# Kernel tuning notes

Measured on AMD Instinct MI355X. Metric: run time of the kernel, lower is better.

Reference implementation:

```python
import jax, jax.numpy as jnp
import numpy as np

B, N, C, H, REG = 1, 2309, 1024, 16, 5
D = C // H


def setup_inputs() -> dict:
    key = jax.random.key(0)
    k0, k1, k2, k3 = jax.random.split(key, 4)
    x = jax.random.normal(k0, (B, N, C), dtype=jnp.float32)
    g_info = jax.random.normal(k1, (12, 2, C), dtype=jnp.float32)
    W_qkv = jax.random.normal(k2, (C, 3 * C), dtype=jnp.float32) * 0.02
    W_proj = jax.random.normal(k3, (C, C), dtype=jnp.float32) * 0.02
    b_proj = jnp.zeros((C,), dtype=jnp.float32)
    return {"x": x, "g_info": g_info, "W_qkv": W_qkv, "W_proj": W_proj, "b_proj": b_proj}


def reference(x, g_info, W_qkv, W_proj, b_proj):
    Bx, Nx, Cx = x.shape
    scale = D ** -0.5
    # qkv projection (qkv_bias=False)
    qkv = (x @ W_qkv).reshape(Bx, Nx, 3, H, D)
    q, k, v = qkv[:, :, 0], qkv[:, :, 1], qkv[:, :, 2]  # [B,N,H,D]

    # grounding query vector from layer 0
    g_layer = g_info[0].reshape(-1, H, D)
    q_g = g_layer[0]  # [H,D]

    # cosine-similarity routing over non-register tokens
    q_pure = q[:, REG:]  # [B,M,H,D]
    q_n = q_pure / jnp.linalg.norm(q_pure, axis=-1, keepdims=True)
    qg_n = q_g / jnp.linalg.norm(q_g, axis=-1, keepdims=True)
    sim = (qg_n[None, None] * q_n).sum(-1).mean(-1)  # [B,M]
    sim = (sim - sim.min()) / (sim.max() - sim.min())  # global min-max normalize
    pos = sim > 0.9  # [B,M] boolean routing mask

    # Full logits computed once; group attention = masked softmax over the
    # group's key set (registers always included). This is mathematically
    # identical to the torch gather->attend->scatter, with static shapes.
    logits = jnp.einsum('bqhd,bkhd->bhqk', q * scale, k)  # [B,H,N,N]

    def masked_attn(tok_mask):
        key_mask = jnp.concatenate([jnp.ones((Bx, REG), bool), tok_mask], axis=1)  # [B,N]
        l = jnp.where(key_mask[:, None, None, :], logits, -jnp.inf)
        a = jax.nn.softmax(l, axis=-1)
        return jnp.einsum('bhqk,bkhd->bqhd', a, v)  # [B,N,H,D]

    x_pos = masked_attn(pos)
    x_neg = masked_attn(~pos)

    reg_out = (x_pos[:, :REG] + x_neg[:, :REG]) * 0.5
    tok_out = jnp.where(pos[:, :, None, None], x_pos[:, REG:], x_neg[:, REG:])
    out = jnp.concatenate([reg_out, tok_out], axis=1).reshape(Bx, Nx, Cx)
    return out @ W_proj + b_proj
```

## Files before the change

### kernel.cpp

```cpp
#include <hip/hip_runtime.h>
#include <math.h>

#define TOK 2309
#define CH 1024
#define NH 16
#define HD 64
#define NREG 5
#define NTOK (TOK - NREG)
#define NPADQ 2432
#define NPAD2 2560
#define NKT 40
#define HTILES 20
#define NQROW 2368
#define QSCL 0.1803368801f

typedef unsigned short ushort_t;
typedef unsigned char uchar_t;
typedef __attribute__((ext_vector_type(8))) short s8frag;
typedef __attribute__((ext_vector_type(4))) float f4frag;
typedef __attribute__((ext_vector_type(2))) long ll2;

__device__ __forceinline__ float wredsum(float v){
  #pragma unroll
  for (int o = 32; o > 0; o >>= 1) v += __shfl_xor(v, o, 64);
  return v;
}

__device__ __forceinline__ unsigned short f2bf(float x){
  union { float f; unsigned u; } v; v.f = x;
  unsigned r = v.u + 0x7FFF + ((v.u >> 16) & 1);
  return (unsigned short)(r >> 16);
}
__device__ __forceinline__ float bf2f(unsigned short u){
  union { unsigned u32; float f; } v; v.u32 = ((unsigned)u) << 16;
  return v.f;
}
__device__ __forceinline__ unsigned pack_bf16(float lo, float hi){
  union { float f; unsigned u; } a, b;
  a.f = lo; b.f = hi;
  return __builtin_amdgcn_perm(b.u + 0x8000u, a.u + 0x8000u, 0x07060302u);
}
__device__ __forceinline__ uchar_t f2fp8(float x){
  return (uchar_t)(__builtin_amdgcn_cvt_pk_fp8_f32(x, x, 0, false) & 0xff);
}
__device__ __forceinline__ void cp16(const void* g, void* l){
  __builtin_amdgcn_global_load_lds(
      (const __attribute__((address_space(1))) unsigned int*)g,
      (__attribute__((address_space(3))) unsigned int*)l, 16, 0, 0);
}

__global__ __launch_bounds__(256) void split_x_kernel(
    const float* __restrict__ X, ushort_t* __restrict__ Xhi, ushort_t* __restrict__ Xlo)
{
  int row = blockIdx.x;
  int c4 = threadIdx.x * 4;
  ushort4 h4 = {0,0,0,0}, l4 = {0,0,0,0};
  if (row < TOK) {
    float4 v = *(const float4*)&X[(size_t)row*CH + c4];
    float vv[4] = {v.x, v.y, v.z, v.w};
    ushort_t hs[4], ls[4];
    #pragma unroll
    for (int i = 0; i < 4; i++) {
      hs[i] = f2bf(vv[i]);
      ls[i] = f2bf(vv[i] - bf2f(hs[i]));
    }
    h4.x=hs[0]; h4.y=hs[1]; h4.z=hs[2]; h4.w=hs[3];
    l4.x=ls[0]; l4.y=ls[1]; l4.z=ls[2]; l4.w=ls[3];
  }
  *(ushort4*)&Xhi[(size_t)row*CH + c4] = h4;
  *(ushort4*)&Xlo[(size_t)row*CH + c4] = l4;
}

__global__ __launch_bounds__(256) void pack_w_kernel(
    const float* __restrict__ W, const int N,
    ushort_t* __restrict__ WT, ushort_t* __restrict__ WloT, const int loN)
{
  __shared__ float T[64][68];
  const int tid = threadIdx.x;
  const int n0 = blockIdx.x * 64;
  const int k0 = blockIdx.y * 64;
  const int lr = tid >> 4;
  const int lc = (tid & 15) * 4;
  #pragma unroll
  for (int s = 0; s < 4; s++) {
    float4 v = *(const float4*)&W[(size_t)(k0 + lr + s*16) * N + n0 + lc];
    *(float4*)&T[lr + s*16][lc] = v;
  }
  __syncthreads();
  const int nl = tid >> 2;
  const int kc = (tid & 3) * 16;
  const bool dolo = (WloT != nullptr) && (n0 < loN);
  ushort_t* dh = WT + (size_t)(n0 + nl) * CH + k0 + kc;
  ushort_t* dl = WloT + (size_t)(n0 + nl) * CH + k0 + kc;
  #pragma unroll
  for (int g = 0; g < 4; g++) {
    float a = T[kc+g*4+0][nl], b = T[kc+g*4+1][nl];
    float c = T[kc+g*4+2][nl], d = T[kc+g*4+3][nl];
    ushort4 oh;
    oh.x=f2bf(a); oh.y=f2bf(b); oh.z=f2bf(c); oh.w=f2bf(d);
    *(ushort4*)&dh[g*4] = oh;
    if (dolo) {
      ushort4 ol;
      ol.x=f2bf(a-bf2f(oh.x)); ol.y=f2bf(b-bf2f(oh.y));
      ol.z=f2bf(c-bf2f(oh.z)); ol.w=f2bf(d-bf2f(oh.w));
      *(ushort4*)&dl[g*4] = ol;
    }
  }
}

__global__ __launch_bounds__(256) void gemm_qkv_mfma(
    const ushort_t* __restrict__ Xhi, const ushort_t* __restrict__ Xlo,
    const ushort_t* __restrict__ WhiT, const ushort_t* __restrict__ WloT,
    float* __restrict__ Qf, uchar_t* __restrict__ Q8,
    uchar_t* __restrict__ K8, ushort_t* __restrict__ Vbf)
{
  __shared__ ushort_t LA[2][2][4096];
  __shared__ ushort_t LB[2][2][4096];
  const int tid = threadIdx.x;
  const int w = tid >> 6, lane = tid & 63;
  const int quad = lane >> 4, c16 = lane & 15;
  const int wm = w >> 1, wn = w & 1;
  const int nt = blockIdx.x, mt = blockIdx.y;
  const int n0 = nt * 128, m0 = mt * 128;
  const bool isQ = (nt < 8);

  const int srow = tid >> 2;
  const int g = (tid & 3) ^ ((tid >> 3) & 3);
  const size_t aoff = (size_t)(m0 + srow)*CH + g*8;
  const size_t boff = (size_t)(n0 + srow)*CH + g*8;
  const int lbase = (tid & 192) * 8;

  f4frag acc[4][4];
  #pragma unroll
  for (int mi = 0; mi < 4; mi++)
    #pragma unroll
    for (int nb = 0; nb < 4; nb++) acc[mi][nb] = (f4frag){0.f,0.f,0.f,0.f};

  const int soff = (quad ^ ((c16 >> 1) & 3)) * 8;
  int aro[4], bro[4];
  #pragma unroll
  for (int i = 0; i < 4; i++) {
    aro[i] = (wm*64 + i*16 + c16)*32 + soff;
    bro[i] = (wn*64 + i*16 + c16)*32 + soff;
  }

#define QKV_STAGE(KT, BUF) {                                                   \
    const int _k = (KT)*32;                                                    \
    cp16(Xhi  + aoff + _k,                 &LA[BUF][0][lbase]);                \
    cp16(Xhi  + aoff + _k + (size_t)64*CH, &LA[BUF][0][2048 + lbase]);         \
    cp16(WhiT + boff + _k,                 &LB[BUF][0][lbase]);                \
    cp16(WhiT + boff + _k + (size_t)64*CH, &LB[BUF][0][2048 + lbase]);         \
    if (isQ) {                                                                 \
      cp16(Xlo  + aoff + _k,                 &LA[BUF][1][lbase]);              \
      cp16(Xlo  + aoff + _k + (size_t)64*CH, &LA[BUF][1][2048 + lbase]);       \
      cp16(WloT + boff + _k,                 &LB[BUF][1][lbase]);              \
      cp16(WloT + boff + _k + (size_t)64*CH, &LB[BUF][1][2048 + lbase]);       \
    } }

  QKV_STAGE(0, 0);
  for (int kt = 0; kt < 32; kt++) {
    const int buf = kt & 1;
    __syncthreads();
    if (kt < 31) { QKV_STAGE(kt+1, buf^1); }
    s8frag a[4], b[4];
    #pragma unroll
    for (int i = 0; i < 4; i++) a[i] = *(const s8frag*)&LA[buf][0][aro[i]];
    #pragma unroll
    for (int i = 0; i < 4; i++) b[i] = *(const s8frag*)&LB[buf][0][bro[i]];
    #pragma unroll
    for (int mi = 0; mi < 4; mi++)
      #pragma unroll
      for (int nb = 0; nb < 4; nb++)
        acc[mi][nb] = __builtin_amdgcn_mfma_f32_16x16x32_bf16(a[mi], b[nb], acc[mi][nb], 0, 0, 0);
    if (isQ) {
      s8frag al[4], bl[4];
      #pragma unroll
      for (int i = 0; i < 4; i++) al[i] = *(const s8frag*)&LA[buf][1][aro[i]];
      #pragma unroll
      for (int i = 0; i < 4; i++) bl[i] = *(const s8frag*)&LB[buf][1][bro[i]];
      #pragma unroll
      for (int mi = 0; mi < 4; mi++)
        #pragma unroll
        for (int nb = 0; nb < 4; nb++) {
          acc[mi][nb] = __builtin_amdgcn_mfma_f32_16x16x32_bf16(a[mi],  bl[nb], acc[mi][nb], 0, 0, 0);
          acc[mi][nb] = __builtin_amdgcn_mfma_f32_16x16x32_bf16(al[mi], b[nb],  acc[mi][nb], 0, 0, 0);
        }
    }
  }
#undef QKV_STAGE

  const int three = (nt >= 16) ? 2 : (nt >= 8) ? 1 : 0;
  #pragma unroll
  for (int mi = 0; mi < 4; mi++) {
    const int orow = m0 + wm*64 + mi*16 + quad*4;
    if (three == 0) {
      #pragma unroll
      for (int nb = 0; nb < 4; nb++) {
        const int col = n0 + wn*64 + nb*16 + c16;
        const int h = (col >> 6) & 15, d = col & 63;
        float* qf = Qf + (size_t)h*TOK*HD;
        uchar_t* q8 = Q8 + (size_t)h*NPADQ*64;
        #pragma unroll
        for (int r = 0; r < 4; r++) {
          int row = orow + r;
          float v = (row < TOK) ? acc[mi][nb][r] : 0.f;
          if (row < TOK) qf[(size_t)row*HD + d] = v;
          q8[(size_t)row*64 + d] = f2fp8(v);
        }
      }
    } else if (three == 1) {
      #pragma unroll
      for (int nb = 0; nb < 4; nb++) {
        const int col = n0 + wn*64 + nb*16 + c16;
        const int h = (col >> 6) & 15;
        const int quadK = ((nb & 1) * 2) + (c16 >> 3);
        const int byteoff = (nb >> 1) * 8 + (c16 & 7);
        uchar_t* base = K8 + (size_t)h*NKT*4096;
        #pragma unroll
        for (int r = 0; r < 4; r++) {
          int row = orow + r;
          float v = (row < TOK) ? acc[mi][nb][r] : 0.f;
          int tile = row >> 6, b = (row >> 4) & 3, c16K = row & 15;
          base[(size_t)tile*4096 + b*1024 + (quadK*16 + c16K)*16 + byteoff] = f2fp8(v);
        }
      }
    } else {
      const int tile  = orow >> 6;
      const int jj    = orow & 63;
      const int c     = jj >> 5;
      const int t16   = (jj >> 4) & 1;
      const int quadA = (jj >> 2) & 3;
      #pragma unroll
      for (int nb = 0; nb < 4; nb++) {
        const int col = n0 + wn*64 + nb*16 + c16;
        const int h = (col >> 6) & 15, d = col & 63;
        const int dblk = d >> 4, c16A = d & 15;
        ushort_t* base = Vbf + (size_t)h*NKT*4096;
        ushort4 o;
        o.x = f2bf((orow+0 < TOK) ? acc[mi][nb][0] : 0.f);
        o.y = f2bf((orow+1 < TOK) ? acc[mi][nb][1] : 0.f);
        o.z = f2bf((orow+2 < TOK) ? acc[mi][nb][2] : 0.f);
        o.w = f2bf((orow+3 < TOK) ? acc[mi][nb][3] : 0.f);
        *(ushort4*)&base[(size_t)tile*4096 + dblk*1024 + c*512
                         + (quadA*16 + c16A)*8 + 4*t16] = o;
      }
    }
  }
}

__global__ __launch_bounds__(256) void sim_kernel(
    const float* __restrict__ Q, const float* __restrict__ G, float* __restrict__ sim)
{
  const int tid = threadIdx.x;
  const int w = tid >> 6, lane = tid & 63;
  float qgn[NH];
  #pragma unroll
  for (int h = 0; h < NH; h++) {
    float g = G[h*HD + lane];
    float n2 = wredsum(g*g);
    qgn[h] = g / sqrtf(n2);
  }
  int it = blockIdx.x * 4 + w;
  if (it >= NTOK) return;
  int i = NREG + it;
  float acc = 0.f;
  #pragma unroll
  for (int h = 0; h < NH; h++) {
    float qv = Q[((size_t)h*TOK + i)*HD + lane];
    float dot = wredsum(qv * qgn[h]);
    float n2  = wredsum(qv * qv);
    acc += dot / sqrtf(n2);
  }
  if (lane == 0) sim[it] = acc * (1.0f/16.0f);
}

__global__ __launch_bounds__(256) void mask_kernel(
    const float* __restrict__ sim, int* __restrict__ cls,
    float* __restrict__ WP, float* __restrict__ WN)
{
  __shared__ float smn[256], smx[256];
  const int tid = threadIdx.x;
  float mn = 1e30f, mx = -1e30f;
  for (int i = tid; i < NTOK; i += 256) { float s = sim[i]; mn = fminf(mn, s); mx = fmaxf(mx, s); }
  smn[tid] = mn; smx[tid] = mx;
  __syncthreads();
  for (int off = 128; off > 0; off >>= 1) {
    if (tid < off) { smn[tid] = fminf(smn[tid], smn[tid+off]); smx[tid] = fmaxf(smx[tid], smx[tid+off]); }
    __syncthreads();
  }
  mn = smn[0]; mx = smx[0];
  float inv = 1.0f / (mx - mn);
  for (int j = tid; j < NPAD2; j += 256) {
    float wp = 0.f, wn = 0.f; int c = 0;
    if (j < NREG) { wp = 1.f; wn = 1.f; c = 2; }
    else if (j < TOK) {
      bool pos = ((sim[j-NREG] - mn) * inv) > 0.9f;
      c = pos ? 1 : 0;
      wp = pos ? 1.f : 0.f;
      wn = pos ? 0.f : 1.f;
    }
    WP[j] = wp; WN[j] = wn;
    if (j < TOK) cls[j] = c;
  }
}

__global__ __launch_bounds__(256) void attn_kernel(
    const uchar_t* __restrict__ Q8, const uchar_t* __restrict__ K8,
    const ushort_t* __restrict__ Vbf,
    const float* __restrict__ WP, const float* __restrict__ WN,
    ushort_t* __restrict__ POp, ushort_t* __restrict__ POn,
    float* __restrict__ Lp, float* __restrict__ Ln)
{
  __shared__ __align__(16) uchar_t smem[24576];
  uchar_t* Kst = smem;
  uchar_t* Vst = smem + 8192;
  const int tid = threadIdx.x;
  const int w = tid >> 6, lane = tid & 63;
  const int quad = lane >> 4, c16 = lane & 15;
  const int h = blockIdx.y;
  const int half = blockIdx.z;
  const int q0 = blockIdx.x * 64;

  const uchar_t* Qh = Q8 + (size_t)h * NPADQ * 64;
  const uchar_t* gk = K8 + ((size_t)h*NKT + half*HTILES)*4096 + tid*16;
  const uchar_t* gv = (const uchar_t*)Vbf + ((size_t)h*NKT + half*HTILES)*8192 + tid*16;
  const int lw = w * 1024;

  const uchar_t* qp = Qh + (size_t)(q0 + w*16 + c16)*64 + quad*8;
  const long qf0 = *(const long*)(qp);
  const long qf1 = *(const long*)(qp + 32);

  f4frag op[4], on[4];
  #pragma unroll
  for (int nb = 0; nb < 4; nb++) { op[nb] = (f4frag){0.f,0.f,0.f,0.f}; on[nb] = (f4frag){0.f,0.f,0.f,0.f}; }
  float lp = 0.f, ln = 0.f;

  cp16(gk, Kst + lw);
  cp16(gv, Vst + lw);
  cp16(gv + 4096, Vst + 4096 + lw);

  int pb = 0;
  for (int t = 0; t < HTILES; t++) {
    __syncthreads();
    if (t < HTILES-1) {
      cp16(gk + (size_t)(t+1)*4096, Kst + (pb^1)*4096 + lw);
      cp16(gv + (size_t)(t+1)*8192,        Vst + (pb^1)*8192 + lw);
      cp16(gv + (size_t)(t+1)*8192 + 4096, Vst + (pb^1)*8192 + 4096 + lw);
    }
    const int j0 = half*(HTILES*64) + t*64;
    f4frag st[4];
    #pragma unroll
    for (int b = 0; b < 4; b++) {
      ll2 kv = *(const ll2*)&Kst[pb*4096 + b*1024 + lane*16];
      f4frag z = (f4frag){0.f,0.f,0.f,0.f};
      z     = __builtin_amdgcn_mfma_f32_16x16x32_fp8_fp8(kv.x, qf0, z, 0, 0, 0);
      st[b] = __builtin_amdgcn_mfma_f32_16x16x32_fp8_fp8(kv.y, qf1, z, 0, 0, 0);
    }
    unsigned pu[4][2], nu[4][2];
    #pragma unroll
    for (int b = 0; b < 4; b++) {
      float4 wp4 = *(const float4*)&WP[j0 + b*16 + quad*4];
      float4 wn4 = *(const float4*)&WN[j0 + b*16 + quad*4];
      float p0 = __builtin_amdgcn_exp2f(st[b][0] * QSCL);
      float p1 = __builtin_amdgcn_exp2f(st[b][1] * QSCL);
      float p2 = __builtin_amdgcn_exp2f(st[b][2] * QSCL);
      float p3 = __builtin_amdgcn_exp2f(st[b][3] * QSCL);
      float a0 = p0*wp4.x, a1 = p1*wp4.y, a2 = p2*wp4.z, a3 = p3*wp4.w;
      float b0 = p0*wn4.x, b1 = p1*wn4.y, b2 = p2*wn4.z, b3 = p3*wn4.w;
      lp += (a0+a1)+(a2+a3);
      ln += (b0+b1)+(b2+b3);
      pu[b][0] = pack_bf16(a0, a1); pu[b][1] = pack_bf16(a2, a3);
      nu[b][0] = pack_bf16(b0, b1); nu[b][1] = pack_bf16(b2, b3);
    }
    union Frag { unsigned u[4]; s8frag v; };
    Frag fp0, fp1, fn0, fn1;
    fp0.u[0]=pu[0][0]; fp0.u[1]=pu[0][1]; fp0.u[2]=pu[1][0]; fp0.u[3]=pu[1][1];
    fp1.u[0]=pu[2][0]; fp1.u[1]=pu[2][1]; fp1.u[2]=pu[3][0]; fp1.u[3]=pu[3][1];
    fn0.u[0]=nu[0][0]; fn0.u[1]=nu[0][1]; fn0.u[2]=nu[1][0]; fn0.u[3]=nu[1][1];
    fn1.u[0]=nu[2][0]; fn1.u[1]=nu[2][1]; fn1.u[2]=nu[3][0]; fn1.u[3]=nu[3][1];
    #pragma unroll
    for (int nb = 0; nb < 4; nb++) {
      s8frag va = *(const s8frag*)&Vst[pb*8192 + nb*2048 + lane*16];
      s8frag vb = *(const s8frag*)&Vst[pb*8192 + nb*2048 + 1024 + lane*16];
      op[nb] = __builtin_amdgcn_mfma_f32_16x16x32_bf16(va, fp0.v, op[nb], 0, 0, 0);
      op[nb] = __builtin_amdgcn_mfma_f32_16x16x32_bf16(vb, fp1.v, op[nb], 0, 0, 0);
      on[nb] = __builtin_amdgcn_mfma_f32_16x16x32_bf16(va, fn0.v, on[nb], 0, 0, 0);
      on[nb] = __builtin_amdgcn_mfma_f32_16x16x32_bf16(vb, fn1.v, on[nb], 0, 0, 0);
    }
    pb ^= 1;
  }

  lp += __shfl_xor(lp, 16, 64); lp += __shfl_xor(lp, 32, 64);
  ln += __shfl_xor(ln, 16, 64); ln += __shfl_xor(ln, 32, 64);
  const int iq = q0 + w*16 + c16;
  if (quad == 0 && iq < TOK) {
    Lp[((size_t)half*NH + h)*NQROW + iq] = lp;
    Ln[((size_t)half*NH + h)*NQROW + iq] = ln;
  }
  if (iq < TOK) {
    const size_t base = (size_t)half*NQROW*CH + (size_t)iq*CH + h*HD;
    #pragma unroll
    for (int nb = 0; nb < 4; nb++) {
      uint2 po, no;
      po.x = pack_bf16(op[nb][0], op[nb][1]);
      po.y = pack_bf16(op[nb][2], op[nb][3]);
      no.x = pack_bf16(on[nb][0], on[nb][1]);
      no.y = pack_bf16(on[nb][2], on[nb][3]);
      *(uint2*)(POp + base + nb*16 + quad*4) = po;
      *(uint2*)(POn + base + nb*16 + quad*4) = no;
    }
  }
}

__global__ __launch_bounds__(256) void merge_kernel(
    const ushort_t* __restrict__ POp, const ushort_t* __restrict__ POn,
    const float* __restrict__ Lp, const float* __restrict__ Ln,
    const int* __restrict__ cls, ushort_t* __restrict__ AObf)
{
  const int row = blockIdx.x;
  const int c4 = threadIdx.x * 4;
  const int h = c4 >> 6;
  const size_t o0 = (size_t)row*CH + c4;
  const size_t o1 = (size_t)NQROW*CH + o0;
  ushort4 p0 = *(const ushort4*)(POp + o0);
  ushort4 p1 = *(const ushort4*)(POp + o1);
  ushort4 n0 = *(const ushort4*)(POn + o0);
  ushort4 n1 = *(const ushort4*)(POn + o1);
  const float lpt = Lp[(size_t)h*NQROW + row] + Lp[(size_t)(NH+h)*NQROW + row];
  const float lnt = Ln[(size_t)h*NQROW + row] + Ln[(size_t)(NH+h)*NQROW + row];
  const float ilp = 1.f / lpt, iln = 1.f / lnt;
  const int cq = cls[row];
  float vp[4], vn[4], o[4];
  vp[0] = (bf2f(p0.x)+bf2f(p1.x))*ilp; vn[0] = (bf2f(n0.x)+bf2f(n1.x))*iln;
  vp[1] = (bf2f(p0.y)+bf2f(p1.y))*ilp; vn[1] = (bf2f(n0.y)+bf2f(n1.y))*iln;
  vp[2] = (bf2f(p0.z)+bf2f(p1.z))*ilp; vn[2] = (bf2f(n0.z)+bf2f(n1.z))*iln;
  vp[3] = (bf2f(p0.w)+bf2f(p1.w))*ilp; vn[3] = (bf2f(n0.w)+bf2f(n1.w))*iln;
  if (row < NREG) {
    #pragma unroll
    for (int i = 0; i < 4; i++) o[i] = 0.5f*(vp[i]+vn[i]);
  } else if (cq == 1) {
    #pragma unroll
    for (int i = 0; i < 4; i++) o[i] = vp[i];
  } else {
    #pragma unroll
    for (int i = 0; i < 4; i++) o[i] = vn[i];
  }
  uint2 pk;
  pk.x = pack_bf16(o[0], o[1]);
  pk.y = pack_bf16(o[2], o[3]);
  *(uint2*)(AObf + (size_t)row*CH + c4) = pk;
}

__global__ __launch_bounds__(256) void gemm_proj_mfma(
    const ushort_t* __restrict__ A, const ushort_t* __restrict__ WT,
    const float* __restrict__ bp, float* __restrict__ out)
{
  __shared__ ushort_t LA[2][4096];
  __shared__ ushort_t LB[2][2048];
  const int tid = threadIdx.x;
  const int w = tid >> 6, lane = tid & 63;
  const int quad = lane >> 4, c16 = lane & 15;
  const int wm = w >> 1, wn = w & 1;
  const int nt = blockIdx.x, mt = blockIdx.y;
  const int n0 = nt * 64, m0 = mt * 128;

  const int srow = tid >> 2;
  const int g = (tid & 3) ^ ((tid >> 3) & 3);
  const size_t aoff = (size_t)(m0 + srow)*CH + g*8;
  const size_t boff = (size_t)(n0 + srow)*CH + g*8;
  const int lbase = (tid & 192) * 8;

  f4frag acc[4][2];
  #pragma unroll
  for (int mi = 0; mi < 4; mi++)
    #pragma unroll
    for (int nb = 0; nb < 2; nb++) acc[mi][nb] = (f4frag){0.f,0.f,0.f,0.f};

  const int soff = (quad ^ ((c16 >> 1) & 3)) * 8;
  int aro[4], bro[2];
  #pragma unroll
  for (int i = 0; i < 4; i++) aro[i] = (wm*64 + i*16 + c16)*32 + soff;
  #pragma unroll
  for (int i = 0; i < 2; i++) bro[i] = (wn*32 + i*16 + c16)*32 + soff;

#define PROJ_STAGE(KT, BUF) {                                                  \
    const int _k = (KT)*32;                                                    \
    cp16(A  + aoff + _k,                 &LA[BUF][lbase]);                     \
    cp16(A  + aoff + _k + (size_t)64*CH, &LA[BUF][2048 + lbase]);              \
    cp16(WT + boff + _k,                 &LB[BUF][lbase]);                     \
    }

  PROJ_STAGE(0, 0);
  for (int kt = 0; kt < 32; kt++) {
    const int buf = kt & 1;
    __syncthreads();
    if (kt < 31) { PROJ_STAGE(kt+1, buf^1); }
    s8frag a[4], b[2];
    #pragma unroll
    for (int i = 0; i < 4; i++) a[i] = *(const s8frag*)&LA[buf][aro[i]];
    #pragma unroll
    for (int i = 0; i < 2; i++) b[i] = *(const s8frag*)&LB[buf][bro[i]];
    #pragma unroll
    for (int mi = 0; mi < 4; mi++)
      #pragma unroll
      for (int nb = 0; nb < 2; nb++)
        acc[mi][nb] = __builtin_amdgcn_mfma_f32_16x16x32_bf16(a[mi], b[nb], acc[mi][nb], 0, 0, 0);
  }
#undef PROJ_STAGE

  #pragma unroll
  for (int mi = 0; mi < 4; mi++) {
    const int orow = m0 + wm*64 + mi*16 + quad*4;
    #pragma unroll
    for (int nb = 0; nb < 2; nb++) {
      const int col = n0 + wn*32 + nb*16 + c16;
      const float bias = bp[col];
      #pragma unroll
      for (int r = 0; r < 4; r++) {
        int row = orow + r;
        if (row < TOK) out[(size_t)row*CH + col] = acc[mi][nb][r] + bias;
      }
    }
  }
}

extern "C" void kernel_launch(void* const* d_in, const int* in_sizes, int n_in,
                              void* d_out, int out_size, void* d_ws, size_t ws_size,
                              hipStream_t stream) {
  const float* x      = (const float*)d_in[0];
  const float* g_info = (const float*)d_in[1];
  const float* W_qkv  = (const float*)d_in[2];
  const float* W_proj = (const float*)d_in[3];
  const float* b_proj = (const float*)d_in[4];
  float* out = (float*)d_out;

  float* ws = (float*)d_ws;
  float* Qf  = ws;
  float* SIM = Qf + (size_t)NH*TOK*HD;
  float* WP  = SIM + NTOK;
  float* WN  = WP + NPAD2;
  int*   CLS = (int*)(WN + NPAD2);
  float* LpB = (float*)(CLS + 2312);
  float* LnB = LpB + (size_t)2*NH*NQROW;
  ushort_t* Xhi    = (ushort_t*)(LnB + (size_t)2*NH*NQROW);
  ushort_t* Xlo    = Xhi    + (size_t)NPADQ*CH;
  ushort_t* WqkvT  = Xlo    + (size_t)NPADQ*CH;
  ushort_t* WqkvLo = WqkvT  + (size_t)3*CH*CH;
  ushort_t* WprojT = WqkvLo + (size_t)CH*CH;
  ushort_t* AObf   = WprojT + (size_t)CH*CH;
  ushort_t* POp    = AObf   + (size_t)NPADQ*CH;
  ushort_t* POn    = POp    + (size_t)2*NQROW*CH;
  uchar_t*  Q8     = (uchar_t*)(POn + (size_t)2*NQROW*CH);
  uchar_t*  K8     = Q8 + (size_t)NH*NPADQ*64;
  ushort_t* Vbf    = (ushort_t*)(K8 + (size_t)NH*NKT*4096);

  hipMemsetAsync(K8, 0, (size_t)NH*NKT*4096 + (size_t)NH*NKT*8192, stream);

  split_x_kernel<<<dim3(NPADQ), 256, 0, stream>>>(x, Xhi, Xlo);
  pack_w_kernel<<<dim3(48, 16), 256, 0, stream>>>(W_qkv, 3*CH, WqkvT, WqkvLo, CH);
  pack_w_kernel<<<dim3(16, 16), 256, 0, stream>>>(W_proj, CH, WprojT, nullptr, 0);
  gemm_qkv_mfma<<<dim3(24, 19), 256, 0, stream>>>(Xhi, Xlo, WqkvT, WqkvLo,
                                                  Qf, Q8, K8, Vbf);
  sim_kernel<<<dim3(576), 256, 0, stream>>>(Qf, g_info, SIM);
  mask_kernel<<<dim3(1), 256, 0, stream>>>(SIM, CLS, WP, WN);
  attn_kernel<<<dim3(37, NH, 2), 256, 0, stream>>>(Q8, K8, Vbf, WP, WN,
                                                   POp, POn, LpB, LnB);
  merge_kernel<<<dim3(TOK), 256, 0, stream>>>(POp, POn, LpB, LnB, CLS, AObf);
  gemm_proj_mfma<<<dim3(16, 19), 256, 0, stream>>>(AObf, WprojT, b_proj, out);
}
```

Before: 257.1 us.

## Drop split-bf16 Q precision, compute routing dot via precomputed W·g projection

```diff
diff --git a/kernel.cpp b/kernel.cpp
--- a/kernel.cpp
+++ b/kernel.cpp
@@ -8,9 +8,9 @@
 #define NREG 5
 #define NTOK (TOK - NREG)
 #define NPADQ 2432
-#define NPAD2 2560
-#define NKT 40
-#define HTILES 20
+#define NPAD2 2432
+#define NKT 38
+#define HTILES 19
 #define NQROW 2368
 #define QSCL 0.1803368801f
 
@@ -20,12 +20,6 @@
 typedef __attribute__((ext_vector_type(4))) float f4frag;
 typedef __attribute__((ext_vector_type(2))) long ll2;
 
-__device__ __forceinline__ float wredsum(float v){
-  #pragma unroll
-  for (int o = 32; o > 0; o >>= 1) v += __shfl_xor(v, o, 64);
-  return v;
-}
-
 __device__ __forceinline__ unsigned short f2bf(float x){
   union { float f; unsigned u; } v; v.f = x;
   unsigned r = v.u + 0x7FFF + ((v.u >> 16) & 1);
@@ -50,34 +44,29 @@
 }
 
 __global__ __launch_bounds__(256) void split_x_kernel(
-    const float* __restrict__ X, ushort_t* __restrict__ Xhi, ushort_t* __restrict__ Xlo)
+    const float* __restrict__ X, ushort_t* __restrict__ Xbf)
 {
   int row = blockIdx.x;
   int c4 = threadIdx.x * 4;
-  ushort4 h4 = {0,0,0,0}, l4 = {0,0,0,0};
+  ushort4 h4 = {0,0,0,0};
   if (row < TOK) {
     float4 v = *(const float4*)&X[(size_t)row*CH + c4];
-    float vv[4] = {v.x, v.y, v.z, v.w};
-    ushort_t hs[4], ls[4];
-    #pragma unroll
-    for (int i = 0; i < 4; i++) {
-      hs[i] = f2bf(vv[i]);
-      ls[i] = f2bf(vv[i] - bf2f(hs[i]));
-    }
-    h4.x=hs[0]; h4.y=hs[1]; h4.z=hs[2]; h4.w=hs[3];
-    l4.x=ls[0]; l4.y=ls[1]; l4.z=ls[2]; l4.w=ls[3];
-  }
-  *(ushort4*)&Xhi[(size_t)row*CH + c4] = h4;
-  *(ushort4*)&Xlo[(size_t)row*CH + c4] = l4;
+    h4.x = f2bf(v.x); h4.y = f2bf(v.y); h4.z = f2bf(v.z); h4.w = f2bf(v.w);
+  }
+  *(ushort4*)&Xbf[(size_t)row*CH + c4] = h4;
 }
 
 __global__ __launch_bounds__(256) void pack_w_kernel(
-    const float* __restrict__ W, const int N,
-    ushort_t* __restrict__ WT, ushort_t* __restrict__ WloT, const int loN)
+    const float* __restrict__ Wqkv, const float* __restrict__ Wproj,
+    ushort_t* __restrict__ WqkvT, ushort_t* __restrict__ WprojT)
 {
   __shared__ float T[64][68];
   const int tid = threadIdx.x;
-  const int n0 = blockIdx.x * 64;
+  int bx = blockIdx.x;
+  const float* W; ushort_t* WT; int N;
+  if (bx < 48) { W = Wqkv; WT = WqkvT; N = 3*CH; }
+  else         { W = Wproj; WT = WprojT; N = CH; bx -= 48; }
+  const int n0 = bx * 64;
   const int k0 = blockIdx.y * 64;
   const int lr = tid >> 4;
   const int lc = (tid & 15) * 4;
@@ -89,40 +78,55 @@
   __syncthreads();
   const int nl = tid >> 2;
   const int kc = (tid & 3) * 16;
-  const bool dolo = (WloT != nullptr) && (n0 < loN);
   ushort_t* dh = WT + (size_t)(n0 + nl) * CH + k0 + kc;
-  ushort_t* dl = WloT + (size_t)(n0 + nl) * CH + k0 + kc;
   #pragma unroll
   for (int g = 0; g < 4; g++) {
-    float a = T[kc+g*4+0][nl], b = T[kc+g*4+1][nl];
-    float c = T[kc+g*4+2][nl], d = T[kc+g*4+3][nl];
     ushort4 oh;
-    oh.x=f2bf(a); oh.y=f2bf(b); oh.z=f2bf(c); oh.w=f2bf(d);
+    oh.x = f2bf(T[kc+g*4+0][nl]); oh.y = f2bf(T[kc+g*4+1][nl]);
+    oh.z = f2bf(T[kc+g*4+2][nl]); oh.w = f2bf(T[kc+g*4+3][nl]);
     *(ushort4*)&dh[g*4] = oh;
-    if (dolo) {
-      ushort4 ol;
-      ol.x=f2bf(a-bf2f(oh.x)); ol.y=f2bf(b-bf2f(oh.y));
-      ol.z=f2bf(c-bf2f(oh.z)); ol.w=f2bf(d-bf2f(oh.w));
-      *(ushort4*)&dl[g*4] = ol;
-    }
-  }
+  }
+}
+
+__global__ __launch_bounds__(256) void ghat_kernel(
+    const float* __restrict__ G, const float* __restrict__ Wqkv,
+    float* __restrict__ U)
+{
+  const int tid = threadIdx.x;
+  const int k = blockIdx.x * 16 + (tid >> 4);
+  const int h = tid & 15;
+  const float* g = G + h*64;
+  float n2 = 0.f;
+  #pragma unroll
+  for (int d = 0; d < 64; d += 4) {
+    float4 gv = *(const float4*)&g[d];
+    n2 += gv.x*gv.x + gv.y*gv.y + gv.z*gv.z + gv.w*gv.w;
+  }
+  const float inv = 1.f / sqrtf(n2);
+  const float* wr = Wqkv + (size_t)k*(3*CH) + h*64;
+  float dot = 0.f;
+  #pragma unroll
+  for (int d = 0; d < 64; d += 4) {
+    float4 wv = *(const float4*)&wr[d];
+    float4 gv = *(const float4*)&g[d];
+    dot += wv.x*gv.x + wv.y*gv.y + wv.z*gv.z + wv.w*gv.w;
+  }
+  U[h*CH + k] = dot * inv;
 }
 
 __global__ __launch_bounds__(256) void gemm_qkv_mfma(
-    const ushort_t* __restrict__ Xhi, const ushort_t* __restrict__ Xlo,
-    const ushort_t* __restrict__ WhiT, const ushort_t* __restrict__ WloT,
-    float* __restrict__ Qf, uchar_t* __restrict__ Q8,
+    const ushort_t* __restrict__ Xbf, const ushort_t* __restrict__ WT,
+    ushort_t* __restrict__ Qbf, uchar_t* __restrict__ Q8,
     uchar_t* __restrict__ K8, ushort_t* __restrict__ Vbf)
 {
-  __shared__ ushort_t LA[2][2][4096];
-  __shared__ ushort_t LB[2][2][4096];
+  __shared__ ushort_t LA[2][4096];
+  __shared__ ushort_t LB[2][4096];
   const int tid = threadIdx.x;
   const int w = tid >> 6, lane = tid & 63;
   const int quad = lane >> 4, c16 = lane & 15;
   const int wm = w >> 1, wn = w & 1;
   const int nt = blockIdx.x, mt = blockIdx.y;
   const int n0 = nt * 128, m0 = mt * 128;
-  const bool isQ = (nt < 8);
 
   const int srow = tid >> 2;
   const int g = (tid & 3) ^ ((tid >> 3) & 3);
@@ -146,16 +150,11 @@
 
 #define QKV_STAGE(KT, BUF) {                                                   \
     const int _k = (KT)*32;                                                    \
-    cp16(Xhi  + aoff + _k,                 &LA[BUF][0][lbase]);                \
-    cp16(Xhi  + aoff + _k + (size_t)64*CH, &LA[BUF][0][2048 + lbase]);         \
-    cp16(WhiT + boff + _k,                 &LB[BUF][0][lbase]);                \
-    cp16(WhiT + boff + _k + (size_t)64*CH, &LB[BUF][0][2048 + lbase]);         \
-    if (isQ) {                                                                 \
-      cp16(Xlo  + aoff + _k,                 &LA[BUF][1][lbase]);              \
-      cp16(Xlo  + aoff + _k + (size_t)64*CH, &LA[BUF][1][2048 + lbase]);       \
-      cp16(WloT + boff + _k,                 &LB[BUF][1][lbase]);              \
-      cp16(WloT + boff + _k + (size_t)64*CH, &LB[BUF][1][2048 + lbase]);       \
-    } }
+    cp16(Xbf + aoff + _k,                 &LA[BUF][lbase]);                    \
+    cp16(Xbf + aoff + _k + (size_t)64*CH, &LA[BUF][2048 + lbase]);             \
+    cp16(WT  + boff + _k,                 &LB[BUF][lbase]);                    \
+    cp16(WT  + boff + _k + (size_t)64*CH, &LB[BUF][2048 + lbase]);             \
+    }
 
   QKV_STAGE(0, 0);
   for (int kt = 0; kt < 32; kt++) {
@@ -164,28 +163,14 @@
     if (kt < 31) { QKV_STAGE(kt+1, buf^1); }
     s8frag a[4], b[4];
     #pragma unroll
-    for (int i = 0; i < 4; i++) a[i] = *(const s8frag*)&LA[buf][0][aro[i]];
-    #pragma unroll
-    for (int i = 0; i < 4; i++) b[i] = *(const s8frag*)&LB[buf][0][bro[i]];
+    for (int i = 0; i < 4; i++) a[i] = *(const s8frag*)&LA[buf][aro[i]];
+    #pragma unroll
+    for (int i = 0; i < 4; i++) b[i] = *(const s8frag*)&LB[buf][bro[i]];
     #pragma unroll
     for (int mi = 0; mi < 4; mi++)
       #pragma unroll
       for (int nb = 0; nb < 4; nb++)
         acc[mi][nb] = __builtin_amdgcn_mfma_f32_16x16x32_bf16(a[mi], b[nb], acc[mi][nb], 0, 0, 0);
-    if (isQ) {
-      s8frag al[4], bl[4];
-      #pragma unroll
-      for (int i = 0; i < 4; i++) al[i] = *(const s8frag*)&LA[buf][1][aro[i]];
-      #pragma unroll
-      for (int i = 0; i < 4; i++) bl[i] = *(const s8frag*)&LB[buf][1][bro[i]];
-      #pragma unroll
-      for (int mi = 0; mi < 4; mi++)
-        #pragma unroll
-        for (int nb = 0; nb < 4; nb++) {
-          acc[mi][nb] = __builtin_amdgcn_mfma_f32_16x16x32_bf16(a[mi],  bl[nb], acc[mi][nb], 0, 0, 0);
-          acc[mi][nb] = __builtin_amdgcn_mfma_f32_16x16x32_bf16(al[mi], b[nb],  acc[mi][nb], 0, 0, 0);
-        }
-    }
   }
 #undef QKV_STAGE
 
@@ -198,13 +183,13 @@
       for (int nb = 0; nb < 4; nb++) {
         const int col = n0 + wn*64 + nb*16 + c16;
         const int h = (col >> 6) & 15, d = col & 63;
-        float* qf = Qf + (size_t)h*TOK*HD;
-        uchar_t* q8 = Q8 + (size_t)h*NPADQ*64;
+        ushort_t* qb = Qbf + (size_t)h*NPADQ*64;
+        uchar_t*  q8 = Q8 + (size_t)h*NPADQ*64;
         #pragma unroll
         for (int r = 0; r < 4; r++) {
           int row = orow + r;
           float v = (row < TOK) ? acc[mi][nb][r] : 0.f;
-          if (row < TOK) qf[(size_t)row*HD + d] = v;
+          qb[(size_t)row*64 + d] = f2bf(v);
           q8[(size_t)row*64 + d] = f2fp8(v);
         }
       }
@@ -219,7 +204,7 @@
         #pragma unroll
         for (int r = 0; r < 4; r++) {
           int row = orow + r;
-          float v = (row < TOK) ? acc[mi][nb][r] : 0.f;
+          float v = (row < TOK) ? acc[mi][nb][r] * QSCL : 0.f;
           int tile = row >> 6, b = (row >> 4) & 3, c16K = row & 15;
           base[(size_t)tile*4096 + b*1024 + (quadK*16 + c16K)*16 + byteoff] = f2fp8(v);
         }
@@ -249,29 +234,35 @@
 }
 
 __global__ __launch_bounds__(256) void sim_kernel(
-    const float* __restrict__ Q, const float* __restrict__ G, float* __restrict__ sim)
-{
-  const int tid = threadIdx.x;
-  const int w = tid >> 6, lane = tid & 63;
-  float qgn[NH];
-  #pragma unroll
-  for (int h = 0; h < NH; h++) {
-    float g = G[h*HD + lane];
-    float n2 = wredsum(g*g);
-    qgn[h] = g / sqrtf(n2);
-  }
-  int it = blockIdx.x * 4 + w;
-  if (it >= NTOK) return;
-  int i = NREG + it;
-  float acc = 0.f;
-  #pragma unroll
-  for (int h = 0; h < NH; h++) {
-    float qv = Q[((size_t)h*TOK + i)*HD + lane];
-    float dot = wredsum(qv * qgn[h]);
-    float n2  = wredsum(qv * qv);
-    acc += dot / sqrtf(n2);
-  }
-  if (lane == 0) sim[it] = acc * (1.0f/16.0f);
+    const float* __restrict__ X, const float* __restrict__ U,
+    const ushort_t* __restrict__ Qbf, float* __restrict__ sim)
+{
+  const int gid = blockIdx.x*256 + threadIdx.x;
+  const int it = gid >> 4;
+  const int h  = gid & 15;
+  const int row = NREG + it;
+  const float* xr = X + (size_t)row*CH;
+  const float* ur = U + h*CH;
+  float num = 0.f;
+  for (int k = 0; k < CH; k += 4) {
+    float4 xv = *(const float4*)&xr[k];
+    float4 uv = *(const float4*)&ur[k];
+    num += xv.x*uv.x + xv.y*uv.y + xv.z*uv.z + xv.w*uv.w;
+  }
+  const ushort_t* qr = Qbf + ((size_t)h*NPADQ + row)*64;
+  float n2 = 0.f;
+  #pragma unroll
+  for (int d = 0; d < 64; d += 4) {
+    ushort4 a = *(const ushort4*)&qr[d];
+    float q0 = bf2f(a.x), q1 = bf2f(a.y), q2 = bf2f(a.z), q3 = bf2f(a.w);
+    n2 += q0*q0 + q1*q1 + q2*q2 + q3*q3;
+  }
+  float acc = num / sqrtf(n2);
+  acc += __shfl_xor(acc, 1, 64);
+  acc += __shfl_xor(acc, 2, 64);
+  acc += __shfl_xor(acc, 4, 64);
+  acc += __shfl_xor(acc, 8, 64);
+  if (h == 0) sim[it] = acc * (1.0f/16.0f);
 }
 
 __global__ __launch_bounds__(256) void mask_kernel(
@@ -361,10 +352,10 @@
     for (int b = 0; b < 4; b++) {
       float4 wp4 = *(const float4*)&WP[j0 + b*16 + quad*4];
       float4 wn4 = *(const float4*)&WN[j0 + b*16 + quad*4];
-      float p0 = __builtin_amdgcn_exp2f(st[b][0] * QSCL);
-      float p1 = __builtin_amdgcn_exp2f(st[b][1] * QSCL);
-      float p2 = __builtin_amdgcn_exp2f(st[b][2] * QSCL);
-      float p3 = __builtin_amdgcn_exp2f(st[b][3] * QSCL);
+      float p0 = __builtin_amdgcn_exp2f(st[b][0]);
+      float p1 = __builtin_amdgcn_exp2f(st[b][1]);
+      float p2 = __builtin_amdgcn_exp2f(st[b][2]);
+      float p3 = __builtin_amdgcn_exp2f(st[b][3]);
       float a0 = p0*wp4.x, a1 = p1*wp4.y, a2 = p2*wp4.z, a3 = p3*wp4.w;
       float b0 = p0*wn4.x, b1 = p1*wn4.y, b2 = p2*wn4.z, b3 = p3*wn4.w;
       lp += (a0+a1)+(a2+a3);
@@ -535,33 +526,29 @@
   float* out = (float*)d_out;
 
   float* ws = (float*)d_ws;
-  float* Qf  = ws;
-  float* SIM = Qf + (size_t)NH*TOK*HD;
+  float* SIM = ws;
   float* WP  = SIM + NTOK;
   float* WN  = WP + NPAD2;
   int*   CLS = (int*)(WN + NPAD2);
   float* LpB = (float*)(CLS + 2312);
   float* LnB = LpB + (size_t)2*NH*NQROW;
-  ushort_t* Xhi    = (ushort_t*)(LnB + (size_t)2*NH*NQROW);
-  ushort_t* Xlo    = Xhi    + (size_t)NPADQ*CH;
-  ushort_t* WqkvT  = Xlo    + (size_t)NPADQ*CH;
-  ushort_t* WqkvLo = WqkvT  + (size_t)3*CH*CH;
-  ushort_t* WprojT = WqkvLo + (size_t)CH*CH;
-  ushort_t* AObf   = WprojT + (size_t)CH*CH;
+  float* U   = LnB + (size_t)2*NH*NQROW;
+  ushort_t* Xbf    = (ushort_t*)(U + (size_t)NH*CH);
+  ushort_t* WqkvT  = Xbf    + (size_t)NPADQ*CH;
+  ushort_t* WprojT = WqkvT  + (size_t)3*CH*CH;
+  ushort_t* Qbf    = WprojT + (size_t)CH*CH;
+  ushort_t* AObf   = Qbf    + (size_t)NH*NPADQ*64;
   ushort_t* POp    = AObf   + (size_t)NPADQ*CH;
   ushort_t* POn    = POp    + (size_t)2*NQROW*CH;
   uchar_t*  Q8     = (uchar_t*)(POn + (size_t)2*NQROW*CH);
   uchar_t*  K8     = Q8 + (size_t)NH*NPADQ*64;
   ushort_t* Vbf    = (ushort_t*)(K8 + (size_t)NH*NKT*4096);
 
-  hipMemsetAsync(K8, 0, (size_t)NH*NKT*4096 + (size_t)NH*NKT*8192, stream);
-
-  split_x_kernel<<<dim3(NPADQ), 256, 0, stream>>>(x, Xhi, Xlo);
-  pack_w_kernel<<<dim3(48, 16), 256, 0, stream>>>(W_qkv, 3*CH, WqkvT, WqkvLo, CH);
-  pack_w_kernel<<<dim3(16, 16), 256, 0, stream>>>(W_proj, CH, WprojT, nullptr, 0);
-  gemm_qkv_mfma<<<dim3(24, 19), 256, 0, stream>>>(Xhi, Xlo, WqkvT, WqkvLo,
-                                                  Qf, Q8, K8, Vbf);
-  sim_kernel<<<dim3(576), 256, 0, stream>>>(Qf, g_info, SIM);
+  split_x_kernel<<<dim3(NPADQ), 256, 0, stream>>>(x, Xbf);
+  pack_w_kernel<<<dim3(64, 16), 256, 0, stream>>>(W_qkv, W_proj, WqkvT, WprojT);
+  ghat_kernel<<<dim3(64), 256, 0, stream>>>(g_info, W_qkv, U);
+  gemm_qkv_mfma<<<dim3(24, 19), 256, 0, stream>>>(Xbf, WqkvT, Qbf, Q8, K8, Vbf);
+  sim_kernel<<<dim3(144), 256, 0, stream>>>(x, U, Qbf, SIM);
   mask_kernel<<<dim3(1), 256, 0, stream>>>(SIM, CLS, WP, WN);
   attn_kernel<<<dim3(37, NH, 2), 256, 0, stream>>>(Q8, K8, Vbf, WP, WN,
                                                    POp, POn, LpB, LnB);
```

Result: slower. 265.0 us (+3.1%).
